# Kernel optimization log

Hardware: AMD Instinct MI355X
Metric: run time of the kernel (lower is better)

## Reference

```python
import jax, jax.numpy as jnp
import numpy as np

LOG2 = 13          # log2_num_embeddings -> K = 8192 codes
TEMP = 1.0         # forward default temperature
BN_EPS = 1e-5

def _codebook_bits():
    ints = jnp.arange(2 ** LOG2)
    bits = (ints[:, None] & (1 << jnp.arange(LOG2 - 1, -1, -1))) > 0
    return bits.astype(jnp.float32)  # [K, LOG2]

def _bn_relu(x, g, b):
    # training-mode BatchNorm1d (biased batch stats) + ReLU
    m = x.mean(axis=0)
    v = x.var(axis=0)
    return jax.nn.relu(g * (x - m) * jax.lax.rsqrt(v + BN_EPS) + b)

def _embed_mlp(bits, w_in, b_in, wh, bh, gammas, betas, w_out, b_out):
    x = _bn_relu(bits @ w_in + b_in, gammas[0], betas[0])
    for i in range(wh.shape[0]):  # 4 hidden blocks (condition_layer=6)
        x = _bn_relu(x @ wh[i] + bh[i], gammas[i + 1], betas[i + 1])
    return x @ w_out + b_out  # [K, vq_dim]

def _normalize(x):
    return x / (jnp.linalg.norm(x, axis=-1, keepdims=True) + 1e-6)

def setup_inputs() -> dict:
    key = jax.random.key(0)
    ks = jax.random.split(key, 8)
    B, L, D, VQ, HID = 4, 2048, 512, 64, 1024
    s = 0.02
    return {
        "h_in": jax.random.normal(ks[0], (B, L, D), jnp.float32),
        "attn_mask": jax.random.randint(ks[1], (B, L), 0, 2, jnp.int32),
        "proj_w": jax.random.normal(ks[2], (D, VQ), jnp.float32) * s,
        "proj_b": jnp.zeros((VQ,), jnp.float32),
        "inv_w": jax.random.normal(ks[3], (VQ, D), jnp.float32) * s,
        "inv_b": jnp.zeros((D,), jnp.float32),
        "mlp_w_in": jax.random.normal(ks[4], (LOG2, HID), jnp.float32) * s,
        "mlp_b_in": jnp.zeros((HID,), jnp.float32),
        "mlp_wh": jax.random.normal(ks[5], (4, HID, HID), jnp.float32) * s,
        "mlp_bh": jnp.zeros((4, HID), jnp.float32),
        "mlp_gammas": jnp.ones((5, HID), jnp.float32),
        "mlp_betas": jnp.zeros((5, HID), jnp.float32),
        "mlp_w_out": jax.random.normal(ks[6], (HID, VQ), jnp.float32) * s,
        "mlp_b_out": jnp.zeros((VQ,), jnp.float32),
    }

def reference(h_in, attn_mask, proj_w, proj_b, inv_w, inv_b,
              mlp_w_in, mlp_b_in, mlp_wh, mlp_bh, mlp_gammas, mlp_betas,
              mlp_w_out, mlp_b_out):
    # project + codebook MLP
    h = h_in @ proj_w + proj_b                                  # [B,L,VQ]
    embed = _embed_mlp(_codebook_bits(), mlp_w_in, mlp_b_in, mlp_wh, mlp_bh,
                       mlp_gammas, mlp_betas, mlp_w_out, mlp_b_out)  # [K,VQ]
    h = _normalize(h)
    embed = _normalize(embed)

    B, L, D = h.shape
    h_flat = h.reshape(B * L, D)
    mask = attn_mask.reshape(-1)                                # int {0,1}
    maskf = mask.astype(h.dtype)

    # attention: distances = -2*(alpha-1)*sg(H C^T) - 2*H C^T ; A = softmax(-d)
    hc = h_flat @ embed.T                                       # [BL,K]
    alpha = 1.0 / TEMP
    distances = -2.0 * (alpha - 1.0) * jax.lax.stop_gradient(hc) - 2.0 * hc
    A = jax.nn.softmax(-distances, axis=1)

    # codebook repulsion loss: max off-diagonal similarity
    mat = embed @ embed.T                                       # [K,K]
    K = mat.shape[0]
    idx = jnp.arange(K)
    mat = mat.at[idx, idx].set(-1.0)
    vq_loss = mat.max(axis=-1).mean()

    # multinomial sample from A == categorical over logits -distances
    code = jax.random.categorical(jax.random.key(1), -distances, axis=-1)
    onehot = jax.nn.one_hot(code, K, dtype=A.dtype)
    # c = onehot - A ; A2 = A + sg(c)  (straight-through one-hot)
    A2 = A + jax.lax.stop_gradient(onehot - A)
    h_vq = h_flat + A2 @ embed - jax.lax.stop_gradient(h_flat)  # [BL,VQ]

    # scatter back into zeros at masked-out positions, then inverse proj
    quantized = (h_vq * maskf[:, None]).reshape(B, L, D)
    quantized = quantized @ inv_w + inv_b                       # [B,L,512]
    vq_code = (code * mask.astype(code.dtype)).reshape(B, L)
    return quantized, vq_code, vq_loss
```

## Files before the change

kernel.cpp:

```cpp
#include <hip/hip_runtime.h>
#include <hip/hip_bf16.h>
#include <stdint.h>

#define HID 1024

__device__ __forceinline__ uint32_t rotl32(uint32_t x, int r) {
  return (x << r) | (x >> (32 - r));
}

__device__ __forceinline__ uint2 threefry2x32_01(uint32_t x0, uint32_t x1) {
  const uint32_t k0 = 0u, k1 = 1u;
  const uint32_t k2 = k0 ^ k1 ^ 0x1BD11BDAu;
  x0 += k0; x1 += k1;
#define TF_R(r) { x0 += x1; x1 = rotl32(x1, r); x1 ^= x0; }
  TF_R(13) TF_R(15) TF_R(26) TF_R(6)
  x0 += k1; x1 += k2 + 1u;
  TF_R(17) TF_R(29) TF_R(16) TF_R(24)
  x0 += k2; x1 += k0 + 2u;
  TF_R(13) TF_R(15) TF_R(26) TF_R(6)
  x0 += k0; x1 += k1 + 3u;
  TF_R(17) TF_R(29) TF_R(16) TF_R(24)
  x0 += k1; x1 += k2 + 4u;
  TF_R(13) TF_R(15) TF_R(26) TF_R(6)
  x0 += k2; x1 += k0 + 5u;
#undef TF_R
  return make_uint2(x0, x1);
}

__device__ __forceinline__ float uni_at(uint32_t flat) {
  uint2 y = threefry2x32_01(0u, flat);
  uint32_t b = y.x ^ y.y;
  float f = __uint_as_float((b >> 9) | 0x3f800000u) - 1.0f;
  return fmaxf(f, 1.17549435e-38f);
}

__device__ __forceinline__ float gumbel_fast(uint32_t flat) {
  float u = uni_at(flat);
  float w = -__logf(u);
  return -__logf(w);
}

__device__ __noinline__ float gumbel_exact(uint32_t flat) {
  float u = uni_at(flat);
  float w = -(float)log((double)u);
  float o = (float)log((double)w);
  return -o;
}

__device__ __forceinline__ float f4c(const float4& v, int i) {
  return i == 0 ? v.x : (i == 1 ? v.y : (i == 2 ? v.z : v.w));
}

__device__ __forceinline__ bool rank_above(float av, int ai, float bv, int bi) {
  return av > bv || (av == bv && ai < bi);
}

template<int BM, int BN_, int BK, int TM, int TN, bool FUSE_BN>
__global__ void __launch_bounds__(256, 4) gemm_bn_relu(
    const float* __restrict__ A, const float* __restrict__ B,
    const float* __restrict__ bias, const float* __restrict__ bna,
    const float* __restrict__ bnc, float* __restrict__ C,
    int M, int N, int K)
{
  __shared__ __align__(16) float As[BK][BM + 4];
  __shared__ __align__(16) float Bs[BK][BN_];
  const int t = threadIdx.x;
  const int n0 = blockIdx.x * BN_;
  const int m0 = blockIdx.y * BM;
  const int tn = t % (BN_ / TN);
  const int tm = t / (BN_ / TN);

  float acc[TM][TN];
#pragma unroll
  for (int i = 0; i < TM; ++i)
#pragma unroll
    for (int j = 0; j < TN; ++j) acc[i][j] = 0.f;

  for (int k0 = 0; k0 < K; k0 += BK) {
    __syncthreads();
#pragma unroll
    for (int p = 0; p < BM * BK / 1024; ++p) {
      int f = t + p * 256;
      int kq = f % (BK / 4);
      int m = f / (BK / 4);
      float4 v = *(const float4*)(A + (size_t)(m0 + m) * K + (k0 + kq * 4));
      if constexpr (FUSE_BN) {
        float4 a4 = *(const float4*)(bna + k0 + kq * 4);
        float4 c4 = *(const float4*)(bnc + k0 + kq * 4);
        v.x = fmaxf(fmaf(v.x, a4.x, c4.x), 0.f);
        v.y = fmaxf(fmaf(v.y, a4.y, c4.y), 0.f);
        v.z = fmaxf(fmaf(v.z, a4.z, c4.z), 0.f);
        v.w = fmaxf(fmaf(v.w, a4.w, c4.w), 0.f);
      }
      As[kq * 4 + 0][m] = v.x;
      As[kq * 4 + 1][m] = v.y;
      As[kq * 4 + 2][m] = v.z;
      As[kq * 4 + 3][m] = v.w;
    }
#pragma unroll
    for (int p = 0; p < BK * BN_ / 1024; ++p) {
      int f = t + p * 256;
      int n4 = f % (BN_ / 4);
      int k = f / (BN_ / 4);
      *(float4*)&Bs[k][n4 * 4] =
          *(const float4*)(B + (size_t)(k0 + k) * N + (n0 + n4 * 4));
    }
    __syncthreads();
#pragma unroll 4
    for (int kk = 0; kk < BK; ++kk) {
      float a[TM], b[TN];
      {
        float4 q0 = *(const float4*)&As[kk][tm * 4];
        a[0] = q0.x; a[1] = q0.y; a[2] = q0.z; a[3] = q0.w;
        if constexpr (TM == 8) {
          float4 q1 = *(const float4*)&As[kk][tm * 4 + BM / 2];
          a[4] = q1.x; a[5] = q1.y; a[6] = q1.z; a[7] = q1.w;
        }
        float4 r0 = *(const float4*)&Bs[kk][tn * 4];
        b[0] = r0.x; b[1] = r0.y; b[2] = r0.z; b[3] = r0.w;
        if constexpr (TN == 8) {
          float4 r1 = *(const float4*)&Bs[kk][tn * 4 + BN_ / 2];
          b[4] = r1.x; b[5] = r1.y; b[6] = r1.z; b[7] = r1.w;
        }
      }
#pragma unroll
      for (int i = 0; i < TM; ++i)
#pragma unroll
        for (int j = 0; j < TN; ++j)
          acc[i][j] = fmaf(a[i], b[j], acc[i][j]);
    }
  }
#pragma unroll
  for (int i = 0; i < TM; ++i) {
    int m = (i < 4) ? (tm * 4 + i) : (tm * 4 + BM / 2 + (i - 4));
#pragma unroll
    for (int jq = 0; jq < TN / 4; ++jq) {
      int n = tn * 4 + jq * (BN_ / 2);
      float4 bv = *(const float4*)(bias + n0 + n);
      float4 o;
      o.x = acc[i][jq * 4 + 0] + bv.x;
      o.y = acc[i][jq * 4 + 1] + bv.y;
      o.z = acc[i][jq * 4 + 2] + bv.z;
      o.w = acc[i][jq * 4 + 3] + bv.w;
      *(float4*)(C + (size_t)(m0 + m) * N + (n0 + n)) = o;
    }
  }
}

__global__ void __launch_bounds__(256) embed_bits_in(
    const float* __restrict__ w_in, const float* __restrict__ b_in,
    float* __restrict__ X)
{
  int k = blockIdx.x;
  int c = threadIdx.x * 4;
  float4 acc = *(const float4*)(b_in + c);
#pragma unroll
  for (int j = 0; j < 13; ++j) {
    if (k & (1 << (12 - j))) {
      float4 w = *(const float4*)(w_in + j * HID + c);
      acc.x += w.x; acc.y += w.y; acc.z += w.z; acc.w += w.w;
    }
  }
  *(float4*)(X + (size_t)k * HID + c) = acc;
}

__global__ void __launch_bounds__(256) bn_stats_partial(
    const float* __restrict__ X, float* __restrict__ part)
{
  int cb = blockIdx.x, rb = blockIdx.y;
  int t = threadIdx.x;
  int cl = t & 31, rs = t >> 5;
  int c = cb * 32 + cl;
  int r0 = rb * 256 + rs * 32;
  float s = 0.f, sq = 0.f;
  const float* p = X + (size_t)r0 * HID + c;
  for (int i = 0; i < 32; ++i) {
    float v = p[(size_t)i * HID];
    s += v;
    sq = fmaf(v, v, sq);
  }
  __shared__ float rs_[8][32], rq_[8][32];
  rs_[rs][cl] = s;
  rq_[rs][cl] = sq;
  __syncthreads();
  if (t < 32) {
    float S = 0.f, Q = 0.f;
    for (int i = 0; i < 8; ++i) { S += rs_[i][t]; Q += rq_[i][t]; }
    size_t o = ((size_t)rb * HID + cb * 32 + t) * 2;
    part[o] = S;
    part[o + 1] = Q;
  }
}

__global__ void __launch_bounds__(256) bn_finalize(
    const float* __restrict__ part, const float* __restrict__ gamma,
    const float* __restrict__ beta, float* __restrict__ bna,
    float* __restrict__ bnc)
{
  int c = blockIdx.x * 256 + threadIdx.x;
  double S = 0.0, Q = 0.0;
  for (int rb = 0; rb < 32; ++rb) {
    size_t o = ((size_t)rb * HID + c) * 2;
    S += (double)part[o];
    Q += (double)part[o + 1];
  }
  double mean = S / 8192.0;
  double var = Q / 8192.0 - mean * mean;
  float r = (float)(1.0 / sqrt(var + 1e-5));
  float a = gamma[c] * r;
  bna[c] = a;
  bnc[c] = fmaf(-(float)mean, a, beta[c]);
}

__global__ void __launch_bounds__(64) row_normalize64(
    const float* __restrict__ in, float* __restrict__ out)
{
  int r = blockIdx.x, t = threadIdx.x;
  float v = in[(size_t)r * 64 + t];
  float ss = v * v;
  for (int m = 32; m >= 1; m >>= 1) ss += __shfl_xor(ss, m);
  float inv = 1.f / (sqrtf(ss) + 1e-6f);
  out[(size_t)r * 64 + t] = v * inv;
}

template<bool GUM>
__global__ void __launch_bounds__(256, 2) score_kernel(
    const float* __restrict__ Arows, const float* __restrict__ eN,
    float* __restrict__ pval, int* __restrict__ pidx)
{
  __shared__ __align__(16) float Ed[64][256];
  __shared__ __align__(16) float Hs[32][64];
  const int t = threadIdx.x;
  const int i0 = (blockIdx.x >> 1) * 32;
  const int kh = blockIdx.x & 1;
  for (int f = t; f < 512; f += 256) {
    int lr = f >> 4, dq = (f & 15) << 2;
    *(float4*)&Hs[lr][dq] = *(const float4*)(Arows + (size_t)(i0 + lr) * 64 + dq);
  }
  const int kg = t & 31;
  const int rg = t >> 5;
  float b1[4], b2[4];
  int i1[4], i2[4];
#pragma unroll
  for (int r = 0; r < 4; ++r) {
    b1[r] = -3.4e38f; b2[r] = -3.4e38f; i1[r] = 0; i2[r] = 0;
  }

  for (int tile = 0; tile < 16; ++tile) {
    const int kb = kh * 4096 + tile * 256;
    __syncthreads();
#pragma unroll
    for (int p = 0; p < 16; ++p) {
      int kk = p * 16 + (t >> 4);
      int dq = (t & 15) << 2;
      float4 v = *(const float4*)(eN + (size_t)(kb + kk) * 64 + dq);
      Ed[dq + 0][kk ^ ((dq + 0) & 28)] = v.x;
      Ed[dq + 1][kk ^ ((dq + 1) & 28)] = v.y;
      Ed[dq + 2][kk ^ ((dq + 2) & 28)] = v.z;
      Ed[dq + 3][kk ^ ((dq + 3) & 28)] = v.w;
    }
    __syncthreads();
    float acc[4][8];
#pragma unroll
    for (int r = 0; r < 4; ++r)
#pragma unroll
      for (int q = 0; q < 8; ++q) acc[r][q] = 0.f;

#pragma unroll 2
    for (int dq = 0; dq < 64; dq += 4) {
      float4 hq[4];
      hq[0] = *(const float4*)&Hs[rg * 4 + 0][dq];
      hq[1] = *(const float4*)&Hs[rg * 4 + 1][dq];
      hq[2] = *(const float4*)&Hs[rg * 4 + 2][dq];
      hq[3] = *(const float4*)&Hs[rg * 4 + 3][dq];
#pragma unroll
      for (int dd = 0; dd < 4; ++dd) {
        const int d = dq + dd;
        const int s = d & 28;
        const float4 ea = *(const float4*)&Ed[d][(kg * 4) ^ s];
        const float4 eb = *(const float4*)&Ed[d][(128 + kg * 4) ^ s];
#pragma unroll
        for (int r = 0; r < 4; ++r) {
          const float hv = f4c(hq[r], dd);
          acc[r][0] = fmaf(hv, ea.x, acc[r][0]);
          acc[r][1] = fmaf(hv, ea.y, acc[r][1]);
          acc[r][2] = fmaf(hv, ea.z, acc[r][2]);
          acc[r][3] = fmaf(hv, ea.w, acc[r][3]);
          acc[r][4] = fmaf(hv, eb.x, acc[r][4]);
          acc[r][5] = fmaf(hv, eb.y, acc[r][5]);
          acc[r][6] = fmaf(hv, eb.z, acc[r][6]);
          acc[r][7] = fmaf(hv, eb.w, acc[r][7]);
        }
      }
    }
#pragma unroll
    for (int r = 0; r < 4; ++r) {
      const uint32_t grow = (uint32_t)(i0 + rg * 4 + r);
#pragma unroll
      for (int q = 0; q < 8; ++q) {
        const int kl = (q < 4) ? (kg * 4 + q) : (128 + kg * 4 + (q - 4));
        const int kgl = kb + kl;
        if constexpr (GUM) {
          float g = gumbel_fast((grow << 13) | (uint32_t)kgl);
          float z = 2.f * acc[r][q] + g;
          if (z > b1[r]) {
            b2[r] = b1[r]; i2[r] = i1[r];
            b1[r] = z; i1[r] = kgl;
          } else if (z > b2[r]) {
            b2[r] = z; i2[r] = kgl;
          }
        } else {
          float z = (kgl == (int)grow) ? -1.0f : acc[r][q];
          if (z > b1[r]) b1[r] = z;
        }
      }
    }
  }
#pragma unroll
  for (int r = 0; r < 4; ++r) {
    if constexpr (GUM) {
      float v1 = b1[r], v2 = b2[r];
      int j1 = i1[r], j2 = i2[r];
      for (int m = 16; m >= 1; m >>= 1) {
        float o1 = __shfl_xor(v1, m), o2 = __shfl_xor(v2, m);
        int p1 = __shfl_xor(j1, m), p2 = __shfl_xor(j2, m);
        if (rank_above(o1, p1, v1, j1)) {
          float nv2; int nj2;
          if (rank_above(v1, j1, o2, p2)) { nv2 = v1; nj2 = j1; }
          else { nv2 = o2; nj2 = p2; }
          v1 = o1; j1 = p1; v2 = nv2; j2 = nj2;
        } else {
          if (rank_above(o1, p1, v2, j2)) { v2 = o1; j2 = p1; }
        }
      }
      if ((t & 31) == 0) {
        const uint32_t grow = (uint32_t)(i0 + rg * 4 + r);
        float g1f = gumbel_fast((grow << 13) | (uint32_t)j1);
        float g1e = gumbel_exact((grow << 13) | (uint32_t)j1);
        float z1 = v1 - g1f + g1e;
        int win = j1;
        if (v1 - v2 <= 1e-3f) {
          float g2f = gumbel_fast((grow << 13) | (uint32_t)j2);
          float g2e = gumbel_exact((grow << 13) | (uint32_t)j2);
          float z2 = v2 - g2f + g2e;
          if (rank_above(z2, j2, z1, win)) { z1 = z2; win = j2; }
        }
        pval[grow * 2 + kh] = z1;
        pidx[grow * 2 + kh] = win;
      }
    } else {
      float bv = b1[r];
      for (int m = 16; m >= 1; m >>= 1) {
        float ov = __shfl_xor(bv, m);
        if (ov > bv) bv = ov;
      }
      if ((t & 31) == 0) {
        int grow = i0 + rg * 4 + r;
        pval[grow * 2 + kh] = bv;
      }
    }
  }
}

__global__ void __launch_bounds__(256) combine_kernel(
    const float* __restrict__ pval, const int* __restrict__ pidx,
    const float* __restrict__ pmax, const int* __restrict__ mask,
    int* __restrict__ codes, float* __restrict__ out_code,
    float* __restrict__ losspart)
{
  int r = blockIdx.x * 256 + threadIdx.x;
  float v0 = pval[r * 2], v1 = pval[r * 2 + 1];
  int code = (v1 > v0) ? pidx[r * 2 + 1] : pidx[r * 2];
  codes[r] = code;
  out_code[r] = (mask[r] != 0) ? (float)code : 0.f;
  float m = fmaxf(pmax[r * 2], pmax[r * 2 + 1]);
  __shared__ float red[256];
  red[threadIdx.x] = m;
  __syncthreads();
  for (int s = 128; s >= 1; s >>= 1) {
    if (threadIdx.x < s) red[threadIdx.x] += red[threadIdx.x + s];
    __syncthreads();
  }
  if (threadIdx.x == 0) losspart[blockIdx.x] = red[0];
}

__global__ void __launch_bounds__(64) loss_final(
    const float* __restrict__ losspart, float* __restrict__ out)
{
  float s = (threadIdx.x < 32) ? losspart[threadIdx.x] : 0.f;
  for (int m = 32; m >= 1; m >>= 1) s += __shfl_xor(s, m);
  if (threadIdx.x == 0) out[0] = s * (1.0f / 8192.0f);
}

__global__ void __launch_bounds__(256, 2) final_proj(
    const float* __restrict__ eN, const int* __restrict__ codes,
    const int* __restrict__ mask, const float* __restrict__ inv_w,
    const float* __restrict__ inv_b, float* __restrict__ out)
{
  __shared__ __align__(16) float Ws[64][128];
  __shared__ __align__(16) float Es[32][64];
  const int t = threadIdx.x;
  const int c0 = blockIdx.x * 128;
  const int r0 = blockIdx.y * 32;
  for (int f = t; f < 512; f += 256) {
    int lr = f >> 4, dq = (f & 15) << 2;
    int grow = r0 + lr;
    float4 v = make_float4(0.f, 0.f, 0.f, 0.f);
    if (mask[grow] != 0)
      v = *(const float4*)(eN + (size_t)codes[grow] * 64 + dq);
    *(float4*)&Es[lr][dq] = v;
  }
  for (int f = t; f < 2048; f += 256) {
    int n4 = f & 31, j = f >> 5;
    *(float4*)&Ws[j][n4 * 4] =
        *(const float4*)(inv_w + (size_t)j * 512 + c0 + n4 * 4);
  }
  __syncthreads();
  const int tx = t & 31, ty = t >> 5;
  float acc[4][4];
#pragma unroll
  for (int r = 0; r < 4; ++r)
#pragma unroll
    for (int j = 0; j < 4; ++j) acc[r][j] = 0.f;
#pragma unroll 4
  for (int j = 0; j < 64; ++j) {
    float4 wv = *(const float4*)&Ws[j][tx * 4];
#pragma unroll
    for (int r = 0; r < 4; ++r) {
      float e = Es[ty * 4 + r][j];
      acc[r][0] = fmaf(e, wv.x, acc[r][0]);
      acc[r][1] = fmaf(e, wv.y, acc[r][1]);
      acc[r][2] = fmaf(e, wv.z, acc[r][2]);
      acc[r][3] = fmaf(e, wv.w, acc[r][3]);
    }
  }
  float4 bv = *(const float4*)(inv_b + c0 + tx * 4);
#pragma unroll
  for (int r = 0; r < 4; ++r) {
    float4 o;
    o.x = acc[r][0] + bv.x;
    o.y = acc[r][1] + bv.y;
    o.z = acc[r][2] + bv.z;
    o.w = acc[r][3] + bv.w;
    *(float4*)(out + (size_t)(r0 + ty * 4 + r) * 512 + c0 + tx * 4) = o;
  }
}

extern "C" void kernel_launch(void* const* d_in, const int* in_sizes, int n_in,
                              void* d_out, int out_size, void* d_ws, size_t ws_size,
                              hipStream_t stream) {
  (void)in_sizes; (void)n_in; (void)out_size; (void)ws_size;
  const float* h_in   = (const float*)d_in[0];
  const int*   mask   = (const int*)d_in[1];
  const float* proj_w = (const float*)d_in[2];
  const float* proj_b = (const float*)d_in[3];
  const float* inv_w  = (const float*)d_in[4];
  const float* inv_b  = (const float*)d_in[5];
  const float* w_in   = (const float*)d_in[6];
  const float* b_in   = (const float*)d_in[7];
  const float* wh     = (const float*)d_in[8];
  const float* bh     = (const float*)d_in[9];
  const float* gam    = (const float*)d_in[10];
  const float* bet    = (const float*)d_in[11];
  const float* w_out  = (const float*)d_in[12];
  const float* b_out  = (const float*)d_in[13];

  float* ws = (float*)d_ws;
  float* XA = ws;
  float* XB = ws + 8388608;
  float* scr = ws + 16777216;
  float* stats   = scr;
  float* pval    = scr;
  int*   pidx    = (int*)(scr + 16384);
  float* pmax    = scr + 32768;
  int*   codes   = (int*)(scr + 49152);
  float* losspart = scr + 57344;
  float* bna = ws + 16842752;
  float* bnc = bna + 1024;
  float* h_norm = ws + 16844800;
  float* e_norm = h_norm + 524288;

  float* out = (float*)d_out;
  float* out_q = out;
  float* out_code = out + 4194304;
  float* out_loss = out + 4202496;

  gemm_bn_relu<64, 64, 32, 4, 4, false><<<dim3(1, 128), 256, 0, stream>>>(
      h_in, proj_w, proj_b, nullptr, nullptr, XB, 8192, 64, 512);
  row_normalize64<<<8192, 64, 0, stream>>>(XB, h_norm);

  embed_bits_in<<<8192, 256, 0, stream>>>(w_in, b_in, XA);
  float* Xcur = XA;
  float* Xnext = XB;
  for (int l = 0; l < 5; ++l) {
    bn_stats_partial<<<dim3(32, 32), 256, 0, stream>>>(Xcur, stats);
    bn_finalize<<<4, 256, 0, stream>>>(stats, gam + l * 1024, bet + l * 1024, bna, bnc);
    if (l < 4) {
      gemm_bn_relu<128, 128, 32, 8, 8, true><<<dim3(8, 64), 256, 0, stream>>>(
          Xcur, wh + (size_t)l * 1024 * 1024, bh + l * 1024, bna, bnc, Xnext,
          8192, 1024, 1024);
      float* tmp = Xcur; Xcur = Xnext; Xnext = tmp;
    } else {
      gemm_bn_relu<64, 64, 32, 4, 4, true><<<dim3(1, 128), 256, 0, stream>>>(
          Xcur, w_out, b_out, bna, bnc, Xnext, 8192, 64, 1024);
    }
  }
  row_normalize64<<<8192, 64, 0, stream>>>(Xnext, e_norm);

  score_kernel<true><<<512, 256, 0, stream>>>(h_norm, e_norm, pval, pidx);
  score_kernel<false><<<512, 256, 0, stream>>>(e_norm, e_norm, pmax, nullptr);

  combine_kernel<<<32, 256, 0, stream>>>(pval, pidx, pmax, mask, codes, out_code, losspart);
  loss_final<<<1, 64, 0, stream>>>(losspart, out_loss);
  final_proj<<<dim3(4, 256), 256, 0, stream>>>(e_norm, codes, mask, inv_w, inv_b, out_q);
}
```

Before: 1.595 ms.

## Enlarge score kernel tile to 64 rows x 512 codes with 4-way code split

The fused distance/argmax score kernel now has each block handle 64 rows against a quarter of the codebook, with each thread accumulating an 8x16 register tile. The codebook is streamed through shared memory in 16-dim chunks, using a padded layout in place of the XOR swizzle. Partial results are split four ways instead of two, and the combine kernel is updated to merge four candidates. Scratch buffers are moved into the reused XA region. The larger register tile increases arithmetic reuse per shared-memory load but raises register pressure and may spill or lower occupancy.

```diff
diff --git a/kernel.cpp b/kernel.cpp
--- a/kernel.cpp
+++ b/kernel.cpp
@@ -228,96 +228,114 @@
     const float* __restrict__ Arows, const float* __restrict__ eN,
     float* __restrict__ pval, int* __restrict__ pidx)
 {
-  __shared__ __align__(16) float Ed[64][256];
-  __shared__ __align__(16) float Hs[32][64];
+  __shared__ __align__(16) float Ed[16][516];
+  __shared__ __align__(16) float Hs[64][68];
   const int t = threadIdx.x;
-  const int i0 = (blockIdx.x >> 1) * 32;
-  const int kh = blockIdx.x & 1;
-  for (int f = t; f < 512; f += 256) {
-    int lr = f >> 4, dq = (f & 15) << 2;
-    *(float4*)&Hs[lr][dq] = *(const float4*)(Arows + (size_t)(i0 + lr) * 64 + dq);
-  }
-  const int kg = t & 31;
-  const int rg = t >> 5;
-  float b1[4], b2[4];
-  int i1[4], i2[4];
-#pragma unroll
-  for (int r = 0; r < 4; ++r) {
-    b1[r] = -3.4e38f; b2[r] = -3.4e38f; i1[r] = 0; i2[r] = 0;
-  }
-
-  for (int tile = 0; tile < 16; ++tile) {
-    const int kb = kh * 4096 + tile * 256;
-    __syncthreads();
-#pragma unroll
-    for (int p = 0; p < 16; ++p) {
-      int kk = p * 16 + (t >> 4);
-      int dq = (t & 15) << 2;
-      float4 v = *(const float4*)(eN + (size_t)(kb + kk) * 64 + dq);
-      Ed[dq + 0][kk ^ ((dq + 0) & 28)] = v.x;
-      Ed[dq + 1][kk ^ ((dq + 1) & 28)] = v.y;
-      Ed[dq + 2][kk ^ ((dq + 2) & 28)] = v.z;
-      Ed[dq + 3][kk ^ ((dq + 3) & 28)] = v.w;
-    }
-    __syncthreads();
-    float acc[4][8];
-#pragma unroll
-    for (int r = 0; r < 4; ++r)
-#pragma unroll
-      for (int q = 0; q < 8; ++q) acc[r][q] = 0.f;
-
-#pragma unroll 2
-    for (int dq = 0; dq < 64; dq += 4) {
-      float4 hq[4];
-      hq[0] = *(const float4*)&Hs[rg * 4 + 0][dq];
-      hq[1] = *(const float4*)&Hs[rg * 4 + 1][dq];
-      hq[2] = *(const float4*)&Hs[rg * 4 + 2][dq];
-      hq[3] = *(const float4*)&Hs[rg * 4 + 3][dq];
-#pragma unroll
-      for (int dd = 0; dd < 4; ++dd) {
-        const int d = dq + dd;
-        const int s = d & 28;
-        const float4 ea = *(const float4*)&Ed[d][(kg * 4) ^ s];
-        const float4 eb = *(const float4*)&Ed[d][(128 + kg * 4) ^ s];
-#pragma unroll
-        for (int r = 0; r < 4; ++r) {
-          const float hv = f4c(hq[r], dd);
-          acc[r][0] = fmaf(hv, ea.x, acc[r][0]);
-          acc[r][1] = fmaf(hv, ea.y, acc[r][1]);
-          acc[r][2] = fmaf(hv, ea.z, acc[r][2]);
-          acc[r][3] = fmaf(hv, ea.w, acc[r][3]);
-          acc[r][4] = fmaf(hv, eb.x, acc[r][4]);
-          acc[r][5] = fmaf(hv, eb.y, acc[r][5]);
-          acc[r][6] = fmaf(hv, eb.z, acc[r][6]);
-          acc[r][7] = fmaf(hv, eb.w, acc[r][7]);
-        }
-      }
-    }
-#pragma unroll
-    for (int r = 0; r < 4; ++r) {
-      const uint32_t grow = (uint32_t)(i0 + rg * 4 + r);
-#pragma unroll
-      for (int q = 0; q < 8; ++q) {
-        const int kl = (q < 4) ? (kg * 4 + q) : (128 + kg * 4 + (q - 4));
-        const int kgl = kb + kl;
-        if constexpr (GUM) {
-          float g = gumbel_fast((grow << 13) | (uint32_t)kgl);
-          float z = 2.f * acc[r][q] + g;
-          if (z > b1[r]) {
-            b2[r] = b1[r]; i2[r] = i1[r];
-            b1[r] = z; i1[r] = kgl;
-          } else if (z > b2[r]) {
-            b2[r] = z; i2[r] = kgl;
+  const int rb = blockIdx.x >> 2;
+  const int kq = blockIdx.x & 3;
+  const int i0 = rb * 64;
+  const int g = t >> 5;
+  const int lane = t & 31;
+  const int r0 = g * 8;
+
+#pragma unroll
+  for (int p = 0; p < 4; ++p) {
+    int f = t + p * 256;
+    int row = f >> 4, ch = (f & 15) * 4;
+    *(float4*)&Hs[row][ch] = *(const float4*)(Arows + (size_t)(i0 + row) * 64 + ch);
+  }
+
+  float b1[8], b2[8];
+  int i1[8], i2[8];
+#pragma unroll
+  for (int r = 0; r < 8; ++r) { b1[r] = -3.4e38f; b2[r] = -3.4e38f; i1[r] = 0; i2[r] = 0; }
+
+  for (int tile = 0; tile < 4; ++tile) {
+    const int kb = kq * 2048 + tile * 512;
+    float acc[8][16];
+#pragma unroll
+    for (int r = 0; r < 8; ++r)
+#pragma unroll
+      for (int q = 0; q < 16; ++q) acc[r][q] = 0.f;
+
+    for (int dc = 0; dc < 4; ++dc) {
+      __syncthreads();
+      {
+        const int kk0 = t >> 2, d4 = (t & 3) * 4;
+#pragma unroll
+        for (int p = 0; p < 8; ++p) {
+          int kk = kk0 + p * 64;
+          float4 v = *(const float4*)(eN + (size_t)(kb + kk) * 64 + dc * 16 + d4);
+          Ed[d4 + 0][kk] = v.x;
+          Ed[d4 + 1][kk] = v.y;
+          Ed[d4 + 2][kk] = v.z;
+          Ed[d4 + 3][kk] = v.w;
+        }
+      }
+      __syncthreads();
+#pragma unroll
+      for (int dq = 0; dq < 4; ++dq) {
+        float4 hq[8];
+#pragma unroll
+        for (int r = 0; r < 8; ++r)
+          hq[r] = *(const float4*)&Hs[r0 + r][dc * 16 + dq * 4];
+#pragma unroll
+        for (int dd = 0; dd < 4; ++dd) {
+          const int d = dq * 4 + dd;
+          float4 ev0 = *(const float4*)&Ed[d][0 * 128 + lane * 4];
+          float4 ev1 = *(const float4*)&Ed[d][1 * 128 + lane * 4];
+          float4 ev2 = *(const float4*)&Ed[d][2 * 128 + lane * 4];
+          float4 ev3 = *(const float4*)&Ed[d][3 * 128 + lane * 4];
+#pragma unroll
+          for (int r = 0; r < 8; ++r) {
+            const float h = f4c(hq[r], dd);
+            acc[r][0]  = fmaf(h, ev0.x, acc[r][0]);
+            acc[r][1]  = fmaf(h, ev0.y, acc[r][1]);
+            acc[r][2]  = fmaf(h, ev0.z, acc[r][2]);
+            acc[r][3]  = fmaf(h, ev0.w, acc[r][3]);
+            acc[r][4]  = fmaf(h, ev1.x, acc[r][4]);
+            acc[r][5]  = fmaf(h, ev1.y, acc[r][5]);
+            acc[r][6]  = fmaf(h, ev1.z, acc[r][6]);
+            acc[r][7]  = fmaf(h, ev1.w, acc[r][7]);
+            acc[r][8]  = fmaf(h, ev2.x, acc[r][8]);
+            acc[r][9]  = fmaf(h, ev2.y, acc[r][9]);
+            acc[r][10] = fmaf(h, ev2.z, acc[r][10]);
+            acc[r][11] = fmaf(h, ev2.w, acc[r][11]);
+            acc[r][12] = fmaf(h, ev3.x, acc[r][12]);
+            acc[r][13] = fmaf(h, ev3.y, acc[r][13]);
+            acc[r][14] = fmaf(h, ev3.z, acc[r][14]);
+            acc[r][15] = fmaf(h, ev3.w, acc[r][15]);
           }
-        } else {
-          float z = (kgl == (int)grow) ? -1.0f : acc[r][q];
-          if (z > b1[r]) b1[r] = z;
-        }
-      }
-    }
-  }
-#pragma unroll
-  for (int r = 0; r < 4; ++r) {
+        }
+      }
+    }
+#pragma unroll
+    for (int r = 0; r < 8; ++r) {
+      const int grow = i0 + r0 + r;
+#pragma unroll
+      for (int j = 0; j < 4; ++j) {
+#pragma unroll
+        for (int e = 0; e < 4; ++e) {
+          const int kgl = kb + j * 128 + lane * 4 + e;
+          if constexpr (GUM) {
+            float gb = gumbel_fast(((uint32_t)grow << 13) | (uint32_t)kgl);
+            float z = fmaf(2.f, acc[r][j * 4 + e], gb);
+            if (z > b1[r]) {
+              b2[r] = b1[r]; i2[r] = i1[r];
+              b1[r] = z; i1[r] = kgl;
+            } else if (z > b2[r]) {
+              b2[r] = z; i2[r] = kgl;
+            }
+          } else {
+            float z = (kgl == grow) ? -1.0f : acc[r][j * 4 + e];
+            if (z > b1[r]) b1[r] = z;
+          }
+        }
+      }
+    }
+  }
+#pragma unroll
+  for (int r = 0; r < 8; ++r) {
     if constexpr (GUM) {
       float v1 = b1[r], v2 = b2[r];
       int j1 = i1[r], j2 = i2[r];
@@ -333,8 +351,8 @@
           if (rank_above(o1, p1, v2, j2)) { v2 = o1; j2 = p1; }
         }
       }
-      if ((t & 31) == 0) {
-        const uint32_t grow = (uint32_t)(i0 + rg * 4 + r);
+      if (lane == 0) {
+        const uint32_t grow = (uint32_t)(i0 + r0 + r);
         float g1f = gumbel_fast((grow << 13) | (uint32_t)j1);
         float g1e = gumbel_exact((grow << 13) | (uint32_t)j1);
         float z1 = v1 - g1f + g1e;
@@ -345,8 +363,8 @@
           float z2 = v2 - g2f + g2e;
           if (rank_above(z2, j2, z1, win)) { z1 = z2; win = j2; }
         }
-        pval[grow * 2 + kh] = z1;
-        pidx[grow * 2 + kh] = win;
+        pval[(size_t)grow * 4 + kq] = z1;
+        pidx[(size_t)grow * 4 + kq] = win;
       }
     } else {
       float bv = b1[r];
@@ -354,9 +372,9 @@
         float ov = __shfl_xor(bv, m);
         if (ov > bv) bv = ov;
       }
-      if ((t & 31) == 0) {
-        int grow = i0 + rg * 4 + r;
-        pval[grow * 2 + kh] = bv;
+      if (lane == 0) {
+        int grow = i0 + r0 + r;
+        pval[(size_t)grow * 4 + kq] = bv;
       }
     }
   }
@@ -369,11 +387,18 @@
     float* __restrict__ losspart)
 {
   int r = blockIdx.x * 256 + threadIdx.x;
-  float v0 = pval[r * 2], v1 = pval[r * 2 + 1];
-  int code = (v1 > v0) ? pidx[r * 2 + 1] : pidx[r * 2];
-  codes[r] = code;
-  out_code[r] = (mask[r] != 0) ? (float)code : 0.f;
-  float m = fmaxf(pmax[r * 2], pmax[r * 2 + 1]);
+  float bv = pval[(size_t)r * 4];
+  int bi = pidx[(size_t)r * 4];
+#pragma unroll
+  for (int p = 1; p < 4; ++p) {
+    float v = pval[(size_t)r * 4 + p];
+    int i = pidx[(size_t)r * 4 + p];
+    if (rank_above(v, i, bv, bi)) { bv = v; bi = i; }
+  }
+  codes[r] = bi;
+  out_code[r] = (mask[r] != 0) ? (float)bi : 0.f;
+  float m = fmaxf(fmaxf(pmax[(size_t)r * 4], pmax[(size_t)r * 4 + 1]),
+                  fmaxf(pmax[(size_t)r * 4 + 2], pmax[(size_t)r * 4 + 3]));
   __shared__ float red[256];
   red[threadIdx.x] = m;
   __syncthreads();
@@ -468,17 +493,17 @@
   float* ws = (float*)d_ws;
   float* XA = ws;
   float* XB = ws + 8388608;
-  float* scr = ws + 16777216;
-  float* stats   = scr;
-  float* pval    = scr;
-  int*   pidx    = (int*)(scr + 16384);
-  float* pmax    = scr + 32768;
-  int*   codes   = (int*)(scr + 49152);
-  float* losspart = scr + 57344;
-  float* bna = ws + 16842752;
+  float* bna = ws + 16777216;
   float* bnc = bna + 1024;
-  float* h_norm = ws + 16844800;
+  float* h_norm = ws + 16779264;
   float* e_norm = h_norm + 524288;
+  float* stats  = e_norm + 524288;
+
+  float* pval    = XA;
+  int*   pidx    = (int*)(XA + 32768);
+  float* pmax    = XA + 65536;
+  int*   codes   = (int*)(XA + 98304);
+  float* losspart = XA + 106496;
 
   float* out = (float*)d_out;
   float* out_q = out;
```

Result: slower. 3.558 ms (+123.1%).
